# Performance work log

Measured on AMD Instinct MI355X. Metric: run time of the kernel, lower is better.

The kernel has to match this reference:

```python
import jax, jax.numpy as jnp
import numpy as np

# Quantum circuit closed form: per wire i, state |0> -> RX(x_i) -> RY(theta_i),
# then <PauliZ_i> = cos(theta_i) * cos(x_i). No entangling gates, so wires are
# independent and the whole per-token loop collapses to one elementwise op.

B, S, E = 8, 4096, 512
NQ, FFN = 8, 2048

def setup_inputs() -> dict:
    key = jax.random.key(0)
    ks = jax.random.split(key, 6)
    return {
        "x": jax.random.normal(ks[0], (B, S, E), dtype=jnp.float32),
        "theta": jax.random.normal(ks[1], (NQ,), dtype=jnp.float32),
        "W1": jax.random.normal(ks[2], (FFN, NQ), dtype=jnp.float32) * (1.0 / np.sqrt(NQ)),
        "b1": jax.random.normal(ks[3], (FFN,), dtype=jnp.float32) * 0.01,
        "W2": jax.random.normal(ks[4], (E, FFN), dtype=jnp.float32) * (1.0 / np.sqrt(FFN)),
        "b2": jax.random.normal(ks[5], (E,), dtype=jnp.float32) * 0.01,
    }

def reference(x, theta, W1, b1, W2, b2):
    n_qubits = theta.shape[0]
    # token_slice = x[:, :, :n_qubits]; <Z> = cos(theta) * cos(x)
    q_out = jnp.cos(x[..., :n_qubits]) * jnp.cos(theta)        # [B, S, NQ]
    h = jax.nn.relu(jnp.einsum('bsq,fq->bsf', q_out, W1) + b1)  # [B, S, FFN]
    out = jnp.einsum('bsf,ef->bse', h, W2) + b2                 # [B, S, E]
    return out
```

## Files before the change

### kernel.cpp

```cpp
#include <hip/hip_runtime.h>
#include <math.h>

typedef __attribute__((ext_vector_type(8)))  short short8;
typedef __attribute__((ext_vector_type(16))) float float16_t;

__device__ __forceinline__ short f2bf(float f) {
    union { float f; unsigned u; } c; c.f = f;
    unsigned u = c.u + 0x7fffu + ((c.u >> 16) & 1u);
    return (short)(u >> 16);
}
__device__ __forceinline__ unsigned fbits(float f) {
    union { float f; unsigned u; } c; c.f = f; return c.u;
}
__device__ __forceinline__ float16_t zero16() {
    float16_t z;
#pragma unroll
    for (int r = 0; r < 16; ++r) z[r] = 0.0f;
    return z;
}

__global__ __launch_bounds__(256) void prep_kernel(
    const float* __restrict__ x, const float* __restrict__ theta,
    const float* __restrict__ W1, const float* __restrict__ b1,
    const float* __restrict__ W2,
    short* __restrict__ W2P, short* __restrict__ Qz, short* __restrict__ W1z)
{
    int gid = blockIdx.x * 256 + threadIdx.x;
    if (gid < 131072) {
        int lane = gid & 63;
        int ks   = (gid >> 6) & 127;
        int nt   = gid >> 13;
        int n = nt * 32 + (lane & 31);
        int k = ks * 16 + (lane >> 5) * 8;
        const float4* p = (const float4*)(W2 + n * 2048 + k);
        float4 v0 = p[0], v1 = p[1];
        short8 o;
        o[0] = f2bf(v0.x); o[1] = f2bf(v0.y); o[2] = f2bf(v0.z); o[3] = f2bf(v0.w);
        o[4] = f2bf(v1.x); o[5] = f2bf(v1.y); o[6] = f2bf(v1.z); o[7] = f2bf(v1.w);
        *(short8*)(W2P + gid * 8) = o;
    } else if (gid < 131072 + 32768) {
        int t = gid - 131072;
        const float4* xp = (const float4*)(x + t * 512);
        float4 x0 = xp[0], x1 = xp[1];
        float xv[8] = {x0.x, x0.y, x0.z, x0.w, x1.x, x1.y, x1.z, x1.w};
        short8 q;
#pragma unroll
        for (int c = 0; c < 8; ++c)
            q[c] = f2bf(cosf(xv[c]) * cosf(theta[c]));
        *(short8*)(Qz + t * 8) = q;
    } else if (gid < 131072 + 32768 + 2048) {
        int f = gid - (131072 + 32768);
        const float4* wp = (const float4*)(W1 + f * 8);
        float4 w0 = wp[0], w1 = wp[1];
        short8 wv;
        wv[0] = f2bf(w0.x); wv[1] = f2bf(w0.y); wv[2] = f2bf(w0.z); wv[3] = f2bf(w0.w);
        wv[4] = f2bf(w1.x); wv[5] = f2bf(w1.y); wv[6] = f2bf(w1.z); wv[7] = f2bf(w1.w);
        short8 bz = {0,0,0,0,0,0,0,0};
        bz[0] = f2bf(b1[f]);
        *(short8*)(W1z + f * 16) = wv;
        *(short8*)(W1z + f * 16 + 8) = bz;
    }
}

__device__ __forceinline__ void stage1_tile(
    short8 a1, const short8* qf, short* __restrict__ dst,
    int wx, int wy, int lh, int l31)
{
#pragma unroll
    for (int i = 0; i < 2; ++i) {
        float16_t d1 = __builtin_amdgcn_mfma_f32_32x32x16_bf16(
            a1, qf[i], zero16(), 0, 0, 0);
        const int m = wy * 64 + i * 32 + l31;
#pragma unroll
        for (int g = 0; g < 4; ++g) {
            float v0 = fmaxf(d1[g * 4 + 0], 0.0f);
            float v1 = fmaxf(d1[g * 4 + 1], 0.0f);
            float v2 = fmaxf(d1[g * 4 + 2], 0.0f);
            float v3 = fmaxf(d1[g * 4 + 3], 0.0f);
            uint2 pp;
            pp.x = __builtin_amdgcn_perm(fbits(v1), fbits(v0), 0x07060302u);
            pp.y = __builtin_amdgcn_perm(fbits(v3), fbits(v2), 0x07060302u);
            *(uint2*)(dst + (wx * 4 + g) * 1024 + m * 8 + 4 * lh) = pp;
        }
    }
}

__global__ __launch_bounds__(256, 2) void ffn_kernel(
    const short* __restrict__ Qz, const short* __restrict__ W1z,
    const short* __restrict__ W2P, const float* __restrict__ b2,
    float* __restrict__ out)
{
    __shared__ short Hs[2 * 8192];

    const int tid  = threadIdx.x;
    const int lane = tid & 63;
    const int w    = tid >> 6;
    const int wy = w & 1, wx = w >> 1;
    const int l31 = lane & 31, lh = lane >> 5;
    const int bid = blockIdx.x;
    const int nt = bid & 1, mt = bid >> 1;
    const int m0 = mt * 128, n0 = nt * 256;

    short8 qf[2];
#pragma unroll
    for (int i = 0; i < 2; ++i) {
        short8 v = {0,0,0,0,0,0,0,0};
        if (lh == 0)
            v = *(const short8*)(Qz + (m0 + wy * 64 + i * 32 + l31) * 8);
        else
            v[0] = (short)0x3F80;
        qf[i] = v;
    }

    int w2off[4];
#pragma unroll
    for (int j = 0; j < 4; ++j)
        w2off[j] = (nt * 8 + wx * 4 + j) * 65536 + lane * 8;
    const int a1off = (wx * 32 + l31) * 16 + lh * 8;

    float16_t acc[2][4];
#pragma unroll
    for (int i = 0; i < 2; ++i)
#pragma unroll
        for (int j = 0; j < 4; ++j) acc[i][j] = zero16();

    const short* W2Pk = W2P;
    const short* W1za = W1z + 2048;

    short8 bfvA[2][4], bfvB[2][4];
#pragma unroll
    for (int ks = 0; ks < 2; ++ks)
#pragma unroll
        for (int j = 0; j < 4; ++j)
            bfvA[ks][j] = *(const short8*)(W2Pk + w2off[j] + ks * 512);
    short8 a1n = *(const short8*)(W1z + 1024 + a1off);
    {
        short8 a1_0 = *(const short8*)(W1z + a1off);
        stage1_tile(a1_0, qf, Hs, wx, wy, lh, l31);
    }
    __syncthreads();

    for (int kt = 0; kt < 32; ++kt) {
        const int p = kt & 1;
        short* wr = Hs + (p ^ 1) * 8192;
        const short* rd = Hs + p * 8192;

#pragma unroll
        for (int ks = 0; ks < 2; ++ks)
#pragma unroll
            for (int j = 0; j < 4; ++j)
                bfvB[ks][j] = *(const short8*)(W2Pk + w2off[j] + (ks + 2) * 512);

        if (kt < 31)
            stage1_tile(a1n, qf, wr, wx, wy, lh, l31);
        if (kt < 30)
            a1n = *(const short8*)(W1za + a1off);
        W1za += 1024;

#pragma unroll
        for (int ks = 0; ks < 2; ++ks) {
            short8 af[2];
#pragma unroll
            for (int i = 0; i < 2; ++i)
                af[i] = *(const short8*)(rd + (ks * 2 + lh) * 1024 +
                                         (wy * 64 + i * 32 + l31) * 8);
#pragma unroll
            for (int i = 0; i < 2; ++i)
#pragma unroll
                for (int j = 0; j < 4; ++j)
                    acc[i][j] = __builtin_amdgcn_mfma_f32_32x32x16_bf16(
                        af[i], bfvA[ks][j], acc[i][j], 0, 0, 0);
        }

        W2Pk += 2048;
        if (kt < 31) {
#pragma unroll
            for (int ks = 0; ks < 2; ++ks)
#pragma unroll
                for (int j = 0; j < 4; ++j)
                    bfvA[ks][j] = *(const short8*)(W2Pk + w2off[j] + ks * 512);
        }

#pragma unroll
        for (int ks = 0; ks < 2; ++ks) {
            short8 af[2];
#pragma unroll
            for (int i = 0; i < 2; ++i)
                af[i] = *(const short8*)(rd + ((ks + 2) * 2 + lh) * 1024 +
                                         (wy * 64 + i * 32 + l31) * 8);
#pragma unroll
            for (int i = 0; i < 2; ++i)
#pragma unroll
                for (int j = 0; j < 4; ++j)
                    acc[i][j] = __builtin_amdgcn_mfma_f32_32x32x16_bf16(
                        af[i], bfvB[ks][j], acc[i][j], 0, 0, 0);
        }

        __syncthreads();
    }

#pragma unroll
    for (int j = 0; j < 4; ++j) {
        const int n = n0 + wx * 128 + j * 32 + l31;
        const float b2v = b2[n];
#pragma unroll
        for (int i = 0; i < 2; ++i) {
            const int base = (m0 + wy * 64 + i * 32 + 4 * lh) * 512 + n;
#pragma unroll
            for (int r = 0; r < 16; ++r) {
                const int off = ((r & 3) + 8 * (r >> 2)) * 512;
                out[base + off] = acc[i][j][r] + b2v;
            }
        }
    }
}

extern "C" void kernel_launch(void* const* d_in, const int* in_sizes, int n_in,
                              void* d_out, int out_size, void* d_ws, size_t ws_size,
                              hipStream_t stream)
{
    const float* x     = (const float*)d_in[0];
    const float* theta = (const float*)d_in[1];
    const float* W1    = (const float*)d_in[2];
    const float* b1    = (const float*)d_in[3];
    const float* W2    = (const float*)d_in[4];
    const float* b2    = (const float*)d_in[5];
    float* out = (float*)d_out;

    short* W2P = (short*)d_ws;
    short* Qz  = (short*)((char*)d_ws + 2097152);
    short* W1z = (short*)((char*)d_ws + 2621440);

    prep_kernel<<<648, 256, 0, stream>>>(x, theta, W1, b1, W2, W2P, Qz, W1z);
    ffn_kernel<<<512, 256, 0, stream>>>(Qz, W1z, W2P, b2, out);
}
```

Before: 175.8 us.

## Double the FFN k-tile per barrier to halve synchronization count

The hidden-layer k-step per main-loop iteration grows from 64 to 128. Each wave now computes two stage-1 tiles into a larger 64 KB double-buffered LDS region, and the W2 fragment prefetch ping-pongs across eight sub-steps. The aim is to halve the number of __syncthreads barriers and loop iterations and give more MFMA work between barriers to hide latency. In exchange, LDS use doubles to 64 KB per block, which may limit the two-blocks-per-CU occupancy and adds register pressure.

Result: slower. 184.5 us (+4.9%).

```diff
diff --git a/kernel.cpp b/kernel.cpp
--- a/kernel.cpp
+++ b/kernel.cpp
@@ -64,7 +64,7 @@
 
 __device__ __forceinline__ void stage1_tile(
     short8 a1, const short8* qf, short* __restrict__ dst,
-    int wx, int wy, int lh, int l31)
+    int cbase, int wy, int lh, int l31)
 {
 #pragma unroll
     for (int i = 0; i < 2; ++i) {
@@ -80,7 +80,7 @@
             uint2 pp;
             pp.x = __builtin_amdgcn_perm(fbits(v1), fbits(v0), 0x07060302u);
             pp.y = __builtin_amdgcn_perm(fbits(v3), fbits(v2), 0x07060302u);
-            *(uint2*)(dst + (wx * 4 + g) * 1024 + m * 8 + 4 * lh) = pp;
+            *(uint2*)(dst + (cbase + g) * 1024 + m * 8 + 4 * lh) = pp;
         }
     }
 }
@@ -90,7 +90,7 @@
     const short* __restrict__ W2P, const float* __restrict__ b2,
     float* __restrict__ out)
 {
-    __shared__ short Hs[2 * 8192];
+    __shared__ short Hs[2 * 16384];
 
     const int tid  = threadIdx.x;
     const int lane = tid & 63;
@@ -116,7 +116,8 @@
 #pragma unroll
     for (int j = 0; j < 4; ++j)
         w2off[j] = (nt * 8 + wx * 4 + j) * 65536 + lane * 8;
-    const int a1off = (wx * 32 + l31) * 16 + lh * 8;
+    const int a1lo = (wx * 64 + l31) * 16 + lh * 8;
+    const int a1hi = a1lo + 512;
 
     float16_t acc[2][4];
 #pragma unroll
@@ -125,7 +126,7 @@
         for (int j = 0; j < 4; ++j) acc[i][j] = zero16();
 
     const short* W2Pk = W2P;
-    const short* W1za = W1z + 2048;
+    const short* W1za = W1z + 4096;
 
     short8 bfvA[2][4], bfvB[2][4];
 #pragma unroll
@@ -133,17 +134,19 @@
 #pragma unroll
         for (int j = 0; j < 4; ++j)
             bfvA[ks][j] = *(const short8*)(W2Pk + w2off[j] + ks * 512);
-    short8 a1n = *(const short8*)(W1z + 1024 + a1off);
+    short8 a1nlo = *(const short8*)(W1z + 2048 + a1lo);
+    short8 a1nhi = *(const short8*)(W1z + 2048 + a1hi);
     {
-        short8 a1_0 = *(const short8*)(W1z + a1off);
-        stage1_tile(a1_0, qf, Hs, wx, wy, lh, l31);
+        short8 lo = *(const short8*)(W1z + a1lo);
+        short8 hi = *(const short8*)(W1z + a1hi);
+        stage1_tile(lo, qf, Hs, wx * 8,     wy, lh, l31);
+        stage1_tile(hi, qf, Hs, wx * 8 + 4, wy, lh, l31);
     }
     __syncthreads();
 
-    for (int kt = 0; kt < 32; ++kt) {
-        const int p = kt & 1;
-        short* wr = Hs + (p ^ 1) * 8192;
-        const short* rd = Hs + p * 8192;
+    for (int kt = 0; kt < 16; ++kt) {
+        short* wr = Hs + ((kt + 1) & 1) * 16384;
+        const short* rd = Hs + (kt & 1) * 16384;
 
 #pragma unroll
         for (int ks = 0; ks < 2; ++ks)
@@ -151,18 +154,22 @@
             for (int j = 0; j < 4; ++j)
                 bfvB[ks][j] = *(const short8*)(W2Pk + w2off[j] + (ks + 2) * 512);
 
-        if (kt < 31)
-            stage1_tile(a1n, qf, wr, wx, wy, lh, l31);
-        if (kt < 30)
-            a1n = *(const short8*)(W1za + a1off);
-        W1za += 1024;
-
-#pragma unroll
-        for (int ks = 0; ks < 2; ++ks) {
-            short8 af[2];
-#pragma unroll
-            for (int i = 0; i < 2; ++i)
-                af[i] = *(const short8*)(rd + (ks * 2 + lh) * 1024 +
+        if (kt < 15) {
+            stage1_tile(a1nlo, qf, wr, wx * 8,     wy, lh, l31);
+            stage1_tile(a1nhi, qf, wr, wx * 8 + 4, wy, lh, l31);
+        }
+        if (kt < 14) {
+            a1nlo = *(const short8*)(W1za + a1lo);
+            a1nhi = *(const short8*)(W1za + a1hi);
+        }
+        W1za += 2048;
+
+#pragma unroll
+        for (int ks = 0; ks < 2; ++ks) {
+            short8 af[2];
+#pragma unroll
+            for (int i = 0; i < 2; ++i)
+                af[i] = *(const short8*)(rd + ((0 + ks) * 2 + lh) * 1024 +
                                          (wy * 64 + i * 32 + l31) * 8);
 #pragma unroll
             for (int i = 0; i < 2; ++i)
@@ -172,8 +179,50 @@
                         af[i], bfvA[ks][j], acc[i][j], 0, 0, 0);
         }
 
-        W2Pk += 2048;
-        if (kt < 31) {
+#pragma unroll
+        for (int ks = 0; ks < 2; ++ks)
+#pragma unroll
+            for (int j = 0; j < 4; ++j)
+                bfvA[ks][j] = *(const short8*)(W2Pk + w2off[j] + (ks + 4) * 512);
+
+#pragma unroll
+        for (int ks = 0; ks < 2; ++ks) {
+            short8 af[2];
+#pragma unroll
+            for (int i = 0; i < 2; ++i)
+                af[i] = *(const short8*)(rd + ((2 + ks) * 2 + lh) * 1024 +
+                                         (wy * 64 + i * 32 + l31) * 8);
+#pragma unroll
+            for (int i = 0; i < 2; ++i)
+#pragma unroll
+                for (int j = 0; j < 4; ++j)
+                    acc[i][j] = __builtin_amdgcn_mfma_f32_32x32x16_bf16(
+                        af[i], bfvB[ks][j], acc[i][j], 0, 0, 0);
+        }
+
+#pragma unroll
+        for (int ks = 0; ks < 2; ++ks)
+#pragma unroll
+            for (int j = 0; j < 4; ++j)
+                bfvB[ks][j] = *(const short8*)(W2Pk + w2off[j] + (ks + 6) * 512);
+
+#pragma unroll
+        for (int ks = 0; ks < 2; ++ks) {
+            short8 af[2];
+#pragma unroll
+            for (int i = 0; i < 2; ++i)
+                af[i] = *(const short8*)(rd + ((4 + ks) * 2 + lh) * 1024 +
+                                         (wy * 64 + i * 32 + l31) * 8);
+#pragma unroll
+            for (int i = 0; i < 2; ++i)
+#pragma unroll
+                for (int j = 0; j < 4; ++j)
+                    acc[i][j] = __builtin_amdgcn_mfma_f32_32x32x16_bf16(
+                        af[i], bfvA[ks][j], acc[i][j], 0, 0, 0);
+        }
+
+        W2Pk += 4096;
+        if (kt < 15) {
 #pragma unroll
             for (int ks = 0; ks < 2; ++ks)
 #pragma unroll
@@ -186,7 +235,7 @@
             short8 af[2];
 #pragma unroll
             for (int i = 0; i < 2; ++i)
-                af[i] = *(const short8*)(rd + ((ks + 2) * 2 + lh) * 1024 +
+                af[i] = *(const short8*)(rd + ((6 + ks) * 2 + lh) * 1024 +
                                          (wy * 64 + i * 32 + l31) * 8);
 #pragma unroll
             for (int i = 0; i < 2; ++i)
```

## Keep hidden activations in registers via lane shuffles, drop LDS staging

Applied to the files above, without the earlier changes.

Removes the shared-memory double buffer for the ReLU hidden tile. Each wave now computes its own 32-row stage-1 tile and rearranges the MFMA output into A-operand layout with cross-half-wave shuffles. This eliminates LDS writes/reads and block barriers. The block tile shrinks from 128x256 to 128x128 with each wave owning 32 rows, and the grid doubles. In exchange, W2 fragment reuse across waves drops (each wave loads its own 4x4 B fragments per k-step with no prefetch), which raises global/L2 traffic. Stage-1 MFMAs are now recomputed per N-block.

Result: slower. 204.1 us (+16.1%).

```diff
diff --git a/kernel.cpp b/kernel.cpp
--- a/kernel.cpp
+++ b/kernel.cpp
@@ -62,155 +62,118 @@
     }
 }
 
-__device__ __forceinline__ void stage1_tile(
-    short8 a1, const short8* qf, short* __restrict__ dst,
-    int wx, int wy, int lh, int l31)
-{
-#pragma unroll
-    for (int i = 0; i < 2; ++i) {
-        float16_t d1 = __builtin_amdgcn_mfma_f32_32x32x16_bf16(
-            a1, qf[i], zero16(), 0, 0, 0);
-        const int m = wy * 64 + i * 32 + l31;
-#pragma unroll
-        for (int g = 0; g < 4; ++g) {
-            float v0 = fmaxf(d1[g * 4 + 0], 0.0f);
-            float v1 = fmaxf(d1[g * 4 + 1], 0.0f);
-            float v2 = fmaxf(d1[g * 4 + 2], 0.0f);
-            float v3 = fmaxf(d1[g * 4 + 3], 0.0f);
-            uint2 pp;
-            pp.x = __builtin_amdgcn_perm(fbits(v1), fbits(v0), 0x07060302u);
-            pp.y = __builtin_amdgcn_perm(fbits(v3), fbits(v2), 0x07060302u);
-            *(uint2*)(dst + (wx * 4 + g) * 1024 + m * 8 + 4 * lh) = pp;
-        }
-    }
-}
-
 __global__ __launch_bounds__(256, 2) void ffn_kernel(
     const short* __restrict__ Qz, const short* __restrict__ W1z,
     const short* __restrict__ W2P, const float* __restrict__ b2,
     float* __restrict__ out)
 {
-    __shared__ short Hs[2 * 8192];
-
     const int tid  = threadIdx.x;
     const int lane = tid & 63;
     const int w    = tid >> 6;
-    const int wy = w & 1, wx = w >> 1;
     const int l31 = lane & 31, lh = lane >> 5;
     const int bid = blockIdx.x;
-    const int nt = bid & 1, mt = bid >> 1;
-    const int m0 = mt * 128, n0 = nt * 256;
+    const int nb = bid & 3, mb = bid >> 2;
+    const int m0 = mb * 128 + w * 32;
+    const int n0 = nb * 128;
 
-    short8 qf[2];
-#pragma unroll
-    for (int i = 0; i < 2; ++i) {
-        short8 v = {0,0,0,0,0,0,0,0};
-        if (lh == 0)
-            v = *(const short8*)(Qz + (m0 + wy * 64 + i * 32 + l31) * 8);
-        else
-            v[0] = (short)0x3F80;
-        qf[i] = v;
-    }
+    short8 qf = {0,0,0,0,0,0,0,0};
+    if (lh == 0)
+        qf = *(const short8*)(Qz + (m0 + l31) * 8);
+    else
+        qf[0] = (short)0x3F80;
 
     int w2off[4];
 #pragma unroll
     for (int j = 0; j < 4; ++j)
-        w2off[j] = (nt * 8 + wx * 4 + j) * 65536 + lane * 8;
-    const int a1off = (wx * 32 + l31) * 16 + lh * 8;
+        w2off[j] = (nb * 4 + j) * 65536 + lane * 8;
+    const int a1off = l31 * 16 + lh * 8;
 
-    float16_t acc[2][4];
+    float16_t acc[4];
 #pragma unroll
-    for (int i = 0; i < 2; ++i)
-#pragma unroll
-        for (int j = 0; j < 4; ++j) acc[i][j] = zero16();
+    for (int j = 0; j < 4; ++j) acc[j] = zero16();
+
+    short8 a1c0 = *(const short8*)(W1z + a1off);
+    short8 a1c1 = *(const short8*)(W1z + 512 + a1off);
+    short8 a1n0 = *(const short8*)(W1z + 1024 + a1off);
+    short8 a1n1 = *(const short8*)(W1z + 1536 + a1off);
+    float16_t d1a = __builtin_amdgcn_mfma_f32_32x32x16_bf16(a1c0, qf, zero16(), 0, 0, 0);
+    float16_t d1b = __builtin_amdgcn_mfma_f32_32x32x16_bf16(a1c1, qf, zero16(), 0, 0, 0);
 
     const short* W2Pk = W2P;
     const short* W1za = W1z + 2048;
 
-    short8 bfvA[2][4], bfvB[2][4];
+    for (int kt = 0; kt < 32; ++kt) {
+        short8 bfv[4][4];
 #pragma unroll
-    for (int ks = 0; ks < 2; ++ks)
-#pragma unroll
-        for (int j = 0; j < 4; ++j)
-            bfvA[ks][j] = *(const short8*)(W2Pk + w2off[j] + ks * 512);
-    short8 a1n = *(const short8*)(W1z + 1024 + a1off);
-    {
-        short8 a1_0 = *(const short8*)(W1z + a1off);
-        stage1_tile(a1_0, qf, Hs, wx, wy, lh, l31);
-    }
-    __syncthreads();
-
-    for (int kt = 0; kt < 32; ++kt) {
-        const int p = kt & 1;
-        short* wr = Hs + (p ^ 1) * 8192;
-        const short* rd = Hs + p * 8192;
-
-#pragma unroll
-        for (int ks = 0; ks < 2; ++ks)
+        for (int ks = 0; ks < 4; ++ks)
 #pragma unroll
             for (int j = 0; j < 4; ++j)
-                bfvB[ks][j] = *(const short8*)(W2Pk + w2off[j] + (ks + 2) * 512);
+                bfv[ks][j] = *(const short8*)(W2Pk + w2off[j] + ks * 512);
 
-        if (kt < 31)
-            stage1_tile(a1n, qf, wr, wx, wy, lh, l31);
-        if (kt < 30)
-            a1n = *(const short8*)(W1za + a1off);
+        unsigned Pw[2][4][2];
+#pragma unroll
+        for (int g = 0; g < 4; ++g) {
+            float a0 = fmaxf(d1a[g * 4 + 0], 0.0f);
+            float a1 = fmaxf(d1a[g * 4 + 1], 0.0f);
+            float a2 = fmaxf(d1a[g * 4 + 2], 0.0f);
+            float a3 = fmaxf(d1a[g * 4 + 3], 0.0f);
+            Pw[0][g][0] = __builtin_amdgcn_perm(fbits(a1), fbits(a0), 0x07060302u);
+            Pw[0][g][1] = __builtin_amdgcn_perm(fbits(a3), fbits(a2), 0x07060302u);
+            float b0 = fmaxf(d1b[g * 4 + 0], 0.0f);
+            float b1 = fmaxf(d1b[g * 4 + 1], 0.0f);
+            float b2v = fmaxf(d1b[g * 4 + 2], 0.0f);
+            float b3 = fmaxf(d1b[g * 4 + 3], 0.0f);
+            Pw[1][g][0] = __builtin_amdgcn_perm(fbits(b1), fbits(b0), 0x07060302u);
+            Pw[1][g][1] = __builtin_amdgcn_perm(fbits(b3), fbits(b2v), 0x07060302u);
+        }
+
+        short8 af[4];
+#pragma unroll
+        for (int ks = 0; ks < 4; ++ks) {
+            const int fh = ks >> 1, e = (ks & 1) * 2;
+            unsigned v1w0 = lh ? Pw[fh][e + 1][0] : Pw[fh][e][0];
+            unsigned v1w1 = lh ? Pw[fh][e + 1][1] : Pw[fh][e][1];
+            unsigned wxw0 = lh ? Pw[fh][e][0] : Pw[fh][e + 1][0];
+            unsigned wxw1 = lh ? Pw[fh][e][1] : Pw[fh][e + 1][1];
+            unsigned p0 = (unsigned)__shfl_xor((int)wxw0, 32, 64);
+            unsigned p1 = (unsigned)__shfl_xor((int)wxw1, 32, 64);
+            union { int4 i4; short8 s8; } u;
+            u.i4.x = (int)(lh ? p0 : v1w0);
+            u.i4.y = (int)(lh ? p1 : v1w1);
+            u.i4.z = (int)(lh ? v1w0 : p0);
+            u.i4.w = (int)(lh ? v1w1 : p1);
+            af[ks] = u.s8;
+        }
+
+        if (kt < 31) {
+            d1a = __builtin_amdgcn_mfma_f32_32x32x16_bf16(a1n0, qf, zero16(), 0, 0, 0);
+            d1b = __builtin_amdgcn_mfma_f32_32x32x16_bf16(a1n1, qf, zero16(), 0, 0, 0);
+        }
+        if (kt < 30) {
+            a1n0 = *(const short8*)(W1za + a1off);
+            a1n1 = *(const short8*)(W1za + 512 + a1off);
+        }
         W1za += 1024;
 
 #pragma unroll
-        for (int ks = 0; ks < 2; ++ks) {
-            short8 af[2];
+        for (int ks = 0; ks < 4; ++ks)
 #pragma unroll
-            for (int i = 0; i < 2; ++i)
-                af[i] = *(const short8*)(rd + (ks * 2 + lh) * 1024 +
-                                         (wy * 64 + i * 32 + l31) * 8);
-#pragma unroll
-            for (int i = 0; i < 2; ++i)
-#pragma unroll
-                for (int j = 0; j < 4; ++j)
-                    acc[i][j] = __builtin_amdgcn_mfma_f32_32x32x16_bf16(
-                        af[i], bfvA[ks][j], acc[i][j], 0, 0, 0);
-        }
+            for (int j = 0; j < 4; ++j)
+                acc[j] = __builtin_amdgcn_mfma_f32_32x32x16_bf16(
+                    af[ks], bfv[ks][j], acc[j], 0, 0, 0);
 
         W2Pk += 2048;
-        if (kt < 31) {
-#pragma unroll
-            for (int ks = 0; ks < 2; ++ks)
-#pragma unroll
-                for (int j = 0; j < 4; ++j)
-                    bfvA[ks][j] = *(const short8*)(W2Pk + w2off[j] + ks * 512);
-        }
-
-#pragma unroll
-        for (int ks = 0; ks < 2; ++ks) {
-            short8 af[2];
-#pragma unroll
-            for (int i = 0; i < 2; ++i)
-                af[i] = *(const short8*)(rd + ((ks + 2) * 2 + lh) * 1024 +
-                                         (wy * 64 + i * 32 + l31) * 8);
-#pragma unroll
-            for (int i = 0; i < 2; ++i)
-#pragma unroll
-                for (int j = 0; j < 4; ++j)
-                    acc[i][j] = __builtin_amdgcn_mfma_f32_32x32x16_bf16(
-                        af[i], bfvB[ks][j], acc[i][j], 0, 0, 0);
-        }
-
-        __syncthreads();
     }
 
 #pragma unroll
     for (int j = 0; j < 4; ++j) {
-        const int n = n0 + wx * 128 + j * 32 + l31;
+        const int n = n0 + j * 32 + l31;
         const float b2v = b2[n];
+        const int base = (m0 + 4 * lh) * 512 + n;
 #pragma unroll
-        for (int i = 0; i < 2; ++i) {
-            const int base = (m0 + wy * 64 + i * 32 + 4 * lh) * 512 + n;
-#pragma unroll
-            for (int r = 0; r < 16; ++r) {
-                const int off = ((r & 3) + 8 * (r >> 2)) * 512;
-                out[base + off] = acc[i][j][r] + b2v;
-            }
+        for (int r = 0; r < 16; ++r) {
+            const int off = ((r & 3) + 8 * (r >> 2)) * 512;
+            out[base + off] = acc[j][r] + b2v;
         }
     }
 }
@@ -232,5 +195,5 @@
     short* W1z = (short*)((char*)d_ws + 2621440);
 
     prep_kernel<<<648, 256, 0, stream>>>(x, theta, W1, b1, W2, W2P, Qz, W1z);
-    ffn_kernel<<<512, 256, 0, stream>>>(Qz, W1z, W2P, b2, out);
+    ffn_kernel<<<1024, 256, 0, stream>>>(Qz, W1z, W2P, b2, out);
 }
```

## Quad-buffer hidden activations to halve barriers and split prep kernel

Applied to the files above, without the earlier changes.

The LDS buffer for the ReLU hidden tile grows from two to four slots. The first-layer MFMA now runs two K-tiles ahead, so the block barrier is needed only every other iteration, which cuts sync stalls in the main GEMM loop. The prep kernel is also split into a W2 repacking launch and a small launch for the cosine features and W1. The price is double the LDS per block, which may reduce occupancy, plus one extra kernel launch.

Result: slower. 181.5 us (+3.3%).

```diff
diff --git a/kernel.cpp b/kernel.cpp
--- a/kernel.cpp
+++ b/kernel.cpp
@@ -19,27 +19,31 @@
     return z;
 }
 
-__global__ __launch_bounds__(256) void prep_kernel(
+__global__ __launch_bounds__(256) void prep_w2p(
+    const float* __restrict__ W2, short* __restrict__ W2P)
+{
+    int gid = blockIdx.x * 256 + threadIdx.x;
+    int lane = gid & 63;
+    int ks   = (gid >> 6) & 127;
+    int nt   = gid >> 13;
+    int n = nt * 32 + (lane & 31);
+    int k = ks * 16 + (lane >> 5) * 8;
+    const float4* p = (const float4*)(W2 + n * 2048 + k);
+    float4 v0 = p[0], v1 = p[1];
+    short8 o;
+    o[0] = f2bf(v0.x); o[1] = f2bf(v0.y); o[2] = f2bf(v0.z); o[3] = f2bf(v0.w);
+    o[4] = f2bf(v1.x); o[5] = f2bf(v1.y); o[6] = f2bf(v1.z); o[7] = f2bf(v1.w);
+    *(short8*)(W2P + gid * 8) = o;
+}
+
+__global__ __launch_bounds__(256) void prep_small(
     const float* __restrict__ x, const float* __restrict__ theta,
     const float* __restrict__ W1, const float* __restrict__ b1,
-    const float* __restrict__ W2,
-    short* __restrict__ W2P, short* __restrict__ Qz, short* __restrict__ W1z)
+    short* __restrict__ Qz, short* __restrict__ W1z)
 {
     int gid = blockIdx.x * 256 + threadIdx.x;
-    if (gid < 131072) {
-        int lane = gid & 63;
-        int ks   = (gid >> 6) & 127;
-        int nt   = gid >> 13;
-        int n = nt * 32 + (lane & 31);
-        int k = ks * 16 + (lane >> 5) * 8;
-        const float4* p = (const float4*)(W2 + n * 2048 + k);
-        float4 v0 = p[0], v1 = p[1];
-        short8 o;
-        o[0] = f2bf(v0.x); o[1] = f2bf(v0.y); o[2] = f2bf(v0.z); o[3] = f2bf(v0.w);
-        o[4] = f2bf(v1.x); o[5] = f2bf(v1.y); o[6] = f2bf(v1.z); o[7] = f2bf(v1.w);
-        *(short8*)(W2P + gid * 8) = o;
-    } else if (gid < 131072 + 32768) {
-        int t = gid - 131072;
+    if (gid < 32768) {
+        int t = gid;
         const float4* xp = (const float4*)(x + t * 512);
         float4 x0 = xp[0], x1 = xp[1];
         float xv[8] = {x0.x, x0.y, x0.z, x0.w, x1.x, x1.y, x1.z, x1.w};
@@ -48,8 +52,8 @@
         for (int c = 0; c < 8; ++c)
             q[c] = f2bf(cosf(xv[c]) * cosf(theta[c]));
         *(short8*)(Qz + t * 8) = q;
-    } else if (gid < 131072 + 32768 + 2048) {
-        int f = gid - (131072 + 32768);
+    } else {
+        int f = gid - 32768;
         const float4* wp = (const float4*)(W1 + f * 8);
         float4 w0 = wp[0], w1 = wp[1];
         short8 wv;
@@ -90,7 +94,7 @@
     const short* __restrict__ W2P, const float* __restrict__ b2,
     float* __restrict__ out)
 {
-    __shared__ short Hs[2 * 8192];
+    __shared__ short Hs[4 * 8192];
 
     const int tid  = threadIdx.x;
     const int lane = tid & 63;
@@ -125,7 +129,6 @@
         for (int j = 0; j < 4; ++j) acc[i][j] = zero16();
 
     const short* W2Pk = W2P;
-    const short* W1za = W1z + 2048;
 
     short8 bfvA[2][4], bfvB[2][4];
 #pragma unroll
@@ -133,17 +136,19 @@
 #pragma unroll
         for (int j = 0; j < 4; ++j)
             bfvA[ks][j] = *(const short8*)(W2Pk + w2off[j] + ks * 512);
-    short8 a1n = *(const short8*)(W1z + 1024 + a1off);
     {
         short8 a1_0 = *(const short8*)(W1z + a1off);
-        stage1_tile(a1_0, qf, Hs, wx, wy, lh, l31);
-    }
+        short8 a1_1 = *(const short8*)(W1z + 1024 + a1off);
+        stage1_tile(a1_0, qf, Hs,        wx, wy, lh, l31);
+        stage1_tile(a1_1, qf, Hs + 8192, wx, wy, lh, l31);
+    }
+    short8 a1n = *(const short8*)(W1z + 2048 + a1off);
+    const short* W1za = W1z + 3 * 1024;
     __syncthreads();
 
     for (int kt = 0; kt < 32; ++kt) {
-        const int p = kt & 1;
-        short* wr = Hs + (p ^ 1) * 8192;
-        const short* rd = Hs + p * 8192;
+        const short* rd = Hs + (kt & 3) * 8192;
+        short* wr = Hs + ((kt + 2) & 3) * 8192;
 
 #pragma unroll
         for (int ks = 0; ks < 2; ++ks)
@@ -151,9 +156,9 @@
             for (int j = 0; j < 4; ++j)
                 bfvB[ks][j] = *(const short8*)(W2Pk + w2off[j] + (ks + 2) * 512);
 
-        if (kt < 31)
+        if (kt < 30)
             stage1_tile(a1n, qf, wr, wx, wy, lh, l31);
-        if (kt < 30)
+        if (kt < 29)
             a1n = *(const short8*)(W1za + a1off);
         W1za += 1024;
 
@@ -196,7 +201,8 @@
                         af[i], bfvB[ks][j], acc[i][j], 0, 0, 0);
         }
 
-        __syncthreads();
+        if (kt & 1)
+            __syncthreads();
     }
 
 #pragma unroll
@@ -231,6 +237,7 @@
     short* Qz  = (short*)((char*)d_ws + 2097152);
     short* W1z = (short*)((char*)d_ws + 2621440);
 
-    prep_kernel<<<648, 256, 0, stream>>>(x, theta, W1, b1, W2, W2P, Qz, W1z);
+    prep_w2p<<<512, 256, 0, stream>>>(W2, W2P);
+    prep_small<<<136, 256, 0, stream>>>(x, theta, W1, b1, Qz, W1z);
     ffn_kernel<<<512, 256, 0, stream>>>(Qz, W1z, W2P, b2, out);
 }
```
